# Optimization experiments

Measured on AMD Instinct MI355X. Metric: run time of the kernel, lower is better.

Reference implementation:

```python
import jax, jax.numpy as jnp
import numpy as np

H, C = 4, 128          # heads, hidden_channels
HC = H * C             # 512
F_IN = 9               # node_feat_dim
G_DIM = 50             # global_feat_dim (20 + 30 MACCS)
N = 30000              # nodes
E = 240000             # edges (before self-loops)
B = 64                 # graphs
EPS_BN = 1e-5
SLOPE = 0.2            # GATv2 LeakyReLU negative slope


def _glorot(key, shape):
    fan_in, fan_out = shape[0], shape[-1]
    lim = (6.0 / (fan_in + fan_out)) ** 0.5
    return jax.random.uniform(key, shape, jnp.float32, -lim, lim)


def setup_inputs() -> dict:
    key = jax.random.key(0)
    ks = jax.random.split(key, 20)
    x = jax.random.normal(ks[0], (N, F_IN), jnp.float32)
    global_feat = jax.random.normal(ks[1], (B, G_DIM), jnp.float32)
    edge_index = jax.random.randint(ks[2], (2, E), 0, N, jnp.int64) if jax.config.jax_enable_x64 else jax.random.randint(ks[2], (2, E), 0, N, jnp.int32)
    batch = jnp.sort(jax.random.randint(ks[3], (N,), 0, B, edge_index.dtype))
    return {
        "x": x, "global_feat": global_feat,
        # GATv2 layer 1
        "W1l": _glorot(ks[4], (F_IN, HC)), "b1l": jnp.zeros((HC,), jnp.float32),
        "W1r": _glorot(ks[5], (F_IN, HC)), "b1r": jnp.zeros((HC,), jnp.float32),
        "att1": _glorot(ks[6], (1, H, C))[0], "bias1": jnp.zeros((HC,), jnp.float32),
        # GATv2 layer 2
        "W2l": _glorot(ks[7], (HC, HC)), "b2l": jnp.zeros((HC,), jnp.float32),
        "W2r": _glorot(ks[8], (HC, HC)), "b2r": jnp.zeros((HC,), jnp.float32),
        "att2": _glorot(ks[9], (1, H, C))[0], "bias2": jnp.zeros((HC,), jnp.float32),
        # BatchNorms
        "bn1_g": jnp.ones((HC,), jnp.float32), "bn1_b": jnp.zeros((HC,), jnp.float32),
        "bn2_g": jnp.ones((HC,), jnp.float32), "bn2_b": jnp.zeros((HC,), jnp.float32),
        # MLP head
        "fc1_w": _glorot(ks[10], (HC + G_DIM, C)), "fc1_b": jnp.zeros((C,), jnp.float32),
        "fc2_w": _glorot(ks[11], (C, 1)), "fc2_b": jnp.zeros((1,), jnp.float32),
        "edge_index": edge_index, "batch": batch,
    }


def gatv2_layer(x, src, dst, Wl, bl, Wr, br, att, bias):
    n = x.shape[0]
    xl = (x @ Wl + bl).reshape(n, H, C)   # source transform
    xr = (x @ Wr + br).reshape(n, H, C)   # target transform
    m = xl[src] + xr[dst]                 # [E, H, C] gathered messages
    e = jnp.sum(jax.nn.leaky_relu(m, SLOPE) * att, axis=-1)  # [E, H]
    # segment softmax over edges grouped by target node
    e_max = jax.ops.segment_max(e, dst, num_segments=n)
    p = jnp.exp(e - e_max[dst])
    denom = jax.ops.segment_sum(p, dst, num_segments=n)
    alpha = p / (denom[dst] + 1e-16)      # [E, H]
    out = jax.ops.segment_sum(alpha[:, :, None] * xl[src], dst, num_segments=n)
    return out.reshape(n, HC) + bias


def batchnorm(x, g, b):
    mu = jnp.mean(x, axis=0)
    var = jnp.mean((x - mu) ** 2, axis=0)  # biased var (torch BN train mode)
    return (x - mu) * jax.lax.rsqrt(var + EPS_BN) * g + b


def reference(x, global_feat, W1l, b1l, W1r, b1r, att1, bias1,
              W2l, b2l, W2r, b2r, att2, bias2,
              bn1_g, bn1_b, bn2_g, bn2_b,
              fc1_w, fc1_b, fc2_w, fc2_b, edge_index, batch):
    n = x.shape[0]
    # add self-loops (PyG GATv2 default)
    loops = jnp.arange(n, dtype=edge_index.dtype)
    src = jnp.concatenate([edge_index[0], loops])
    dst = jnp.concatenate([edge_index[1], loops])

    h = gatv2_layer(x, src, dst, W1l, b1l, W1r, b1r, att1, bias1)
    h = jax.nn.relu(batchnorm(h, bn1_g, bn1_b))
    h = gatv2_layer(h, src, dst, W2l, b2l, W2r, b2r, att2, bias2)
    h = jax.nn.relu(batchnorm(h, bn2_g, bn2_b))

    # global mean pool over graphs
    sums = jax.ops.segment_sum(h, batch, num_segments=B)
    counts = jax.ops.segment_sum(jnp.ones((n, 1), h.dtype), batch, num_segments=B)
    pooled = sums / jnp.maximum(counts, 1.0)

    z = jnp.concatenate([pooled, global_feat], axis=1)
    z = jax.nn.relu(z @ fc1_w + fc1_b)  # dropout is identity in eval
    return jnp.squeeze(z @ fc2_w + fc2_b, axis=-1)
```

## Files before the change

kernel.cpp:

```cpp
#include <hip/hip_runtime.h>
#include <math.h>

#define NHEAD 4
#define CCH 128
#define HCD 512
#define SLOPE 0.2f
#define EPS_BN 1e-5f

typedef short s8v __attribute__((ext_vector_type(8)));
typedef float f32x4 __attribute__((ext_vector_type(4)));

__device__ __forceinline__ unsigned short f2bf(float f) {
    unsigned int u = __float_as_uint(f);
    return (unsigned short)((u + 0x7FFFu + ((u >> 16) & 1u)) >> 16);
}
__device__ __forceinline__ float bf2f(unsigned short b) {
    return __uint_as_float(((unsigned int)b) << 16);
}

__global__ void lin1_kernel(const float* __restrict__ x,
                            const float* __restrict__ Wl, const float* __restrict__ bl,
                            const float* __restrict__ Wr, const float* __restrict__ br,
                            float* __restrict__ xl, float* __restrict__ xr, int n) {
    int gid = blockIdx.x * blockDim.x + threadIdx.x;
    if (gid >= n * HCD) return;
    int node = gid >> 9;
    int c = gid & (HCD - 1);
    const float* xrow = x + node * 9;
    float a = bl[c], bz = br[c];
#pragma unroll
    for (int k = 0; k < 9; ++k) {
        float xv = xrow[k];
        a  = fmaf(xv, Wl[k * HCD + c], a);
        bz = fmaf(xv, Wr[k * HCD + c], bz);
    }
    xl[gid] = a;
    xr[gid] = bz;
}

__global__ void splitA_kernel(const float* __restrict__ h,
                              const float* __restrict__ scale, const float* __restrict__ shift,
                              unsigned short* __restrict__ Ah, unsigned short* __restrict__ Al,
                              int total4) {
    int gid = blockIdx.x * blockDim.x + threadIdx.x;
    if (gid >= total4) return;
    int c4 = gid & 127;
    float4 v = ((const float4*)h)[gid];
    float4 sc = ((const float4*)scale)[c4];
    float4 sh = ((const float4*)shift)[c4];
    float f0 = fmaxf(fmaf(v.x, sc.x, sh.x), 0.f);
    float f1 = fmaxf(fmaf(v.y, sc.y, sh.y), 0.f);
    float f2 = fmaxf(fmaf(v.z, sc.z, sh.z), 0.f);
    float f3 = fmaxf(fmaf(v.w, sc.w, sh.w), 0.f);
    unsigned short h0 = f2bf(f0), h1 = f2bf(f1), h2 = f2bf(f2), h3 = f2bf(f3);
    short4 hv = make_short4((short)h0, (short)h1, (short)h2, (short)h3);
    short4 lv = make_short4((short)f2bf(f0 - bf2f(h0)), (short)f2bf(f1 - bf2f(h1)),
                            (short)f2bf(f2 - bf2f(h2)), (short)f2bf(f3 - bf2f(h3)));
    ((short4*)Ah)[gid] = hv;
    ((short4*)Al)[gid] = lv;
}

__global__ void splitBT_kernel(const float* __restrict__ Wl, const float* __restrict__ Wr,
                               unsigned short* __restrict__ BThl, unsigned short* __restrict__ BTll,
                               unsigned short* __restrict__ BThr, unsigned short* __restrict__ BTlr) {
    int gid = blockIdx.x * blockDim.x + threadIdx.x;
    int col = gid >> 9;
    int k = gid & 511;
    float vl = Wl[k * HCD + col];
    float vr = Wr[k * HCD + col];
    unsigned short hl = f2bf(vl);
    unsigned short hr = f2bf(vr);
    BThl[gid] = hl; BTll[gid] = f2bf(vl - bf2f(hl));
    BThr[gid] = hr; BTlr[gid] = f2bf(vr - bf2f(hr));
}

__global__ __launch_bounds__(256) void gemm_mfma_kernel(
        const unsigned short* __restrict__ Ah, const unsigned short* __restrict__ Al,
        const unsigned short* __restrict__ BThL, const unsigned short* __restrict__ BTlL,
        const unsigned short* __restrict__ BThR, const unsigned short* __restrict__ BTlR,
        const float* __restrict__ biasl, const float* __restrict__ biasr,
        float* __restrict__ outL, float* __restrict__ outR, int M) {
    __shared__ short sAh[4096], sAl[4096], sBh[4096], sBl[4096];
    const int nrt = gridDim.x >> 3;
    const int bphys = blockIdx.x;
    const int l = (bphys & 7) * nrt + (bphys >> 3);
    const int y = l & 7;
    const int row0 = (l >> 3) * 128;
    const unsigned short* BTh = (y < 4) ? BThL : BThR;
    const unsigned short* BTl = (y < 4) ? BTlL : BTlR;
    const float* bias = (y < 4) ? biasl : biasr;
    float* C = (y < 4) ? outL : outR;
    const int col0 = (y & 3) * 128;
    const int tid  = threadIdx.x;
    const int wave = tid >> 6;
    const int lane = tid & 63;
    const int str = tid >> 2;
    const int skb = tid & 3;

    f32x4 acc[4][4];
#pragma unroll
    for (int i = 0; i < 4; ++i)
#pragma unroll
        for (int j = 0; j < 4; ++j) acc[i][j] = (f32x4){0.f, 0.f, 0.f, 0.f};

    const int abase = (wave & 1) * 2048;
    const int bbase = (wave >> 1) * 2048;
    const int rkb = lane >> 4;
    const int rrow = (lane & 15) ^ (rkb << 1);
    const int roff = rkb * 128 + rrow * 8;

    s8v pAh[2], pAl[2], pBh[2], pBl[2];
    const s8v zero8 = (s8v){0,0,0,0,0,0,0,0};

#define GLOAD(k0)                                                                     \
    {                                                                                 \
        _Pragma("unroll")                                                             \
        for (int cc = 0; cc < 2; ++cc) {                                              \
            int r = str + cc * 64;                                                    \
            if (row0 + r < M) {                                                       \
                pAh[cc] = *(const s8v*)(Ah + (size_t)(row0 + r) * 512 + (k0) + skb * 8); \
                pAl[cc] = *(const s8v*)(Al + (size_t)(row0 + r) * 512 + (k0) + skb * 8); \
            } else { pAh[cc] = zero8; pAl[cc] = zero8; }                              \
            pBh[cc] = *(const s8v*)(BTh + (size_t)(col0 + r) * 512 + (k0) + skb * 8); \
            pBl[cc] = *(const s8v*)(BTl + (size_t)(col0 + r) * 512 + (k0) + skb * 8); \
        }                                                                             \
    }

    GLOAD(0);
    for (int k0 = 0; k0 < 512; k0 += 32) {
        __syncthreads();
#pragma unroll
        for (int cc = 0; cc < 2; ++cc) {
            int r = str + cc * 64;
            int idx = (r >> 4) * 512 + skb * 128 + (((r & 15) ^ (skb << 1)) * 8);
            *(s8v*)&sAh[idx] = pAh[cc];
            *(s8v*)&sAl[idx] = pAl[cc];
            *(s8v*)&sBh[idx] = pBh[cc];
            *(s8v*)&sBl[idx] = pBl[cc];
        }
        __syncthreads();
        if (k0 + 32 < 512) GLOAD(k0 + 32);
#pragma unroll
        for (int sr = 0; sr < 4; ++sr) {
            s8v ah = *(const s8v*)&sAh[abase + sr * 512 + roff];
            s8v al = *(const s8v*)&sAl[abase + sr * 512 + roff];
#pragma unroll
            for (int sc = 0; sc < 4; ++sc) {
                s8v bh = *(const s8v*)&sBh[bbase + sc * 512 + roff];
                s8v bl = *(const s8v*)&sBl[bbase + sc * 512 + roff];
                acc[sr][sc] = __builtin_amdgcn_mfma_f32_16x16x32_bf16(ah, bh, acc[sr][sc], 0, 0, 0);
                acc[sr][sc] = __builtin_amdgcn_mfma_f32_16x16x32_bf16(al, bh, acc[sr][sc], 0, 0, 0);
                acc[sr][sc] = __builtin_amdgcn_mfma_f32_16x16x32_bf16(ah, bl, acc[sr][sc], 0, 0, 0);
            }
        }
    }
#undef GLOAD
    const int crow = row0 + (wave & 1) * 64;
    const int ccol = col0 + (wave >> 1) * 64;
#pragma unroll
    for (int sr = 0; sr < 4; ++sr) {
        int rbase = crow + sr * 16 + ((lane >> 4) << 2);
#pragma unroll
        for (int sc = 0; sc < 4; ++sc) {
            int col = ccol + sc * 16 + (lane & 15);
            float bb = bias[col];
#pragma unroll
            for (int j = 0; j < 4; ++j) {
                int r = rbase + j;
                if (r < M) C[(size_t)r * 512 + col] = acc[sr][sc][j] + bb;
            }
        }
    }
}


__global__ void hist_kernel(const int* __restrict__ edst, int* __restrict__ deg, int E, int Etot) {
    int e = blockIdx.x * blockDim.x + threadIdx.x;
    if (e >= Etot) return;
    int dst = (e < E) ? edst[e] : (e - E);
    atomicAdd(&deg[dst], 1);
}

__global__ __launch_bounds__(1024) void scan_kernel(const int* __restrict__ deg,
                                                    int* __restrict__ rowstart, int n) {
    __shared__ int buf[1024];
    __shared__ int carry;
    if (threadIdx.x == 0) carry = 0;
    __syncthreads();
    for (int base = 0; base < n; base += 1024) {
        int i = base + (int)threadIdx.x;
        int v = (i < n) ? deg[i] : 0;
        buf[threadIdx.x] = v;
        __syncthreads();
        for (int off = 1; off < 1024; off <<= 1) {
            int t = (threadIdx.x >= (unsigned)off) ? buf[threadIdx.x - off] : 0;
            __syncthreads();
            buf[threadIdx.x] += t;
            __syncthreads();
        }
        if (i < n) rowstart[i] = carry + buf[threadIdx.x] - v;
        int blocksum = buf[1023];
        __syncthreads();
        if (threadIdx.x == 0) carry += blocksum;
        __syncthreads();
    }
    if (threadIdx.x == 0) rowstart[n] = carry;
}

__global__ void scatter_kernel(const int* __restrict__ esrc, const int* __restrict__ edst,
                               const int* __restrict__ rowstart, int* __restrict__ cursor,
                               int* __restrict__ s_src, int E, int Etot) {
    int e = blockIdx.x * blockDim.x + threadIdx.x;
    if (e >= Etot) return;
    int src = (e < E) ? esrc[e] : (e - E);
    int dst = (e < E) ? edst[e] : (e - E);
    int pos = rowstart[dst] + atomicAdd(&cursor[dst], 1);
    s_src[pos] = src;
}

__global__ __launch_bounds__(256) void gat_fused_kernel(
        const float* __restrict__ xl, const float* __restrict__ xr,
        const float* __restrict__ att,
        const int* __restrict__ rowstart, const int* __restrict__ s_src,
        float* __restrict__ out) {
    int node = blockIdx.x;
    int h    = threadIdx.x >> 6;
    int lane = threadIdx.x & 63;
    int beg = rowstart[node];
    int end = rowstart[node + 1];
    int c0 = h * CCH + (lane << 1);
    float2 r2 = *(const float2*)(xr + (size_t)node * HCD + c0);
    float2 a2 = *(const float2*)(att + c0);
    float m = -3.0e38f, den = 0.f, acc0 = 0.f, acc1 = 0.f;

    int j = beg;
    float2 q0, q1, q2, q3;
    q0 = *(const float2*)(xl + (size_t)s_src[j] * HCD + c0);
    if (j + 1 < end) q1 = *(const float2*)(xl + (size_t)s_src[j + 1] * HCD + c0);
    if (j + 2 < end) q2 = *(const float2*)(xl + (size_t)s_src[j + 2] * HCD + c0);
    if (j + 3 < end) q3 = *(const float2*)(xl + (size_t)s_src[j + 3] * HCD + c0);

    while (j + 1 < end) {
        float2 A = q0, B = q1;
        q0 = q2; q1 = q3;
        if (j + 4 < end) q2 = *(const float2*)(xl + (size_t)s_src[j + 4] * HCD + c0);
        if (j + 5 < end) q3 = *(const float2*)(xl + (size_t)s_src[j + 5] * HCD + c0);
        float ta0 = A.x + r2.x; ta0 = (ta0 > 0.f) ? ta0 : SLOPE * ta0;
        float ta1 = A.y + r2.y; ta1 = (ta1 > 0.f) ? ta1 : SLOPE * ta1;
        float tb0 = B.x + r2.x; tb0 = (tb0 > 0.f) ? tb0 : SLOPE * tb0;
        float tb1 = B.y + r2.y; tb1 = (tb1 > 0.f) ? tb1 : SLOPE * tb1;
        float sA = fmaf(ta0, a2.x, ta1 * a2.y);
        float sB = fmaf(tb0, a2.x, tb1 * a2.y);
#pragma unroll
        for (int k = 1; k < 64; k <<= 1) {
            sA += __shfl_xor(sA, k);
            sB += __shfl_xor(sB, k);
        }
        float mn = fmaxf(m, fmaxf(sA, sB));
        float sc = expf(m - mn);
        float pA = expf(sA - mn);
        float pB = expf(sB - mn);
        den  = fmaf(den,  sc, pA + pB);
        acc0 = fmaf(acc0, sc, fmaf(pA, A.x, pB * B.x));
        acc1 = fmaf(acc1, sc, fmaf(pA, A.y, pB * B.y));
        m = mn;
        j += 2;
    }
    if (j < end) {
        float2 A = q0;
        float ta0 = A.x + r2.x; ta0 = (ta0 > 0.f) ? ta0 : SLOPE * ta0;
        float ta1 = A.y + r2.y; ta1 = (ta1 > 0.f) ? ta1 : SLOPE * ta1;
        float sA = fmaf(ta0, a2.x, ta1 * a2.y);
#pragma unroll
        for (int k = 1; k < 64; k <<= 1) sA += __shfl_xor(sA, k);
        float mn = fmaxf(m, sA);
        float sc = expf(m - mn);
        float pA = expf(sA - mn);
        den  = fmaf(den,  sc, pA);
        acc0 = fmaf(acc0, sc, pA * A.x);
        acc1 = fmaf(acc1, sc, pA * A.y);
    }
    float inv = 1.0f / (den + 1e-16f);
    *(float2*)(out + (size_t)node * HCD + c0) = make_float2(acc0 * inv, acc1 * inv);
}

__global__ void bn_stats_kernel(const float* __restrict__ h, float* __restrict__ sum,
                                float* __restrict__ sumsq, int n) {
    int c = blockIdx.y * blockDim.x + threadIdx.x;
    int r0 = blockIdx.x * 128;
    int r1 = min(r0 + 128, n);
    float s = 0.f, s2 = 0.f;
    for (int r = r0; r < r1; ++r) {
        float v = h[(size_t)r * HCD + c];
        s += v;
        s2 = fmaf(v, v, s2);
    }
    atomicAdd(&sum[c], s);
    atomicAdd(&sumsq[c], s2);
}

__global__ void bn_finalize_kernel(const float* __restrict__ sum, const float* __restrict__ sumsq,
                                   const float* __restrict__ g, const float* __restrict__ b,
                                   float* __restrict__ scale, float* __restrict__ shift, int n) {
    int c = threadIdx.x;
    float inv_n = 1.0f / (float)n;
    float mu = sum[c] * inv_n;
    float var = fmaxf(sumsq[c] * inv_n - mu * mu, 0.0f);
    float sc = g[c] * rsqrtf(var + EPS_BN);
    scale[c] = sc;
    shift[c] = b[c] - mu * sc;
}

__device__ __forceinline__ int lower_bound_i(const int* __restrict__ a, int n, int key) {
    int lo = 0, hi = n;
    while (lo < hi) {
        int mid = (lo + hi) >> 1;
        if (a[mid] < key) lo = mid + 1; else hi = mid;
    }
    return lo;
}

__global__ void pool_bnrelu_kernel(const float* __restrict__ h, const int* __restrict__ batch,
                                   const float* __restrict__ scale, const float* __restrict__ shift,
                                   float* __restrict__ pooled, int n) {
    int g = blockIdx.x;
    int c = threadIdx.x;
    int start = lower_bound_i(batch, n, g);
    int end   = lower_bound_i(batch, n, g + 1);
    float sc = scale[c], sh = shift[c];
    float s = 0.f;
    for (int r = start; r < end; ++r)
        s += fmaxf(fmaf(h[(size_t)r * HCD + c], sc, sh), 0.f);
    float cnt = (float)max(end - start, 1);
    pooled[(size_t)g * HCD + c] = s / cnt;
}

__global__ void head_kernel(const float* __restrict__ pooled, const float* __restrict__ gfeat,
                            const float* __restrict__ fc1w, const float* __restrict__ fc1b,
                            const float* __restrict__ fc2w, const float* __restrict__ fc2b,
                            float* __restrict__ out, int gdim) {
    int g = blockIdx.x;
    int j = threadIdx.x;
    float acc = fc1b[j];
    const float* prow = pooled + (size_t)g * HCD;
    for (int i = 0; i < HCD; ++i) acc = fmaf(prow[i], fc1w[i * CCH + j], acc);
    const float* grow = gfeat + (size_t)g * gdim;
    for (int i = 0; i < gdim; ++i) acc = fmaf(grow[i], fc1w[(HCD + i) * CCH + j], acc);
    acc = fmaxf(acc, 0.f);
    __shared__ float z[CCH];
    z[j] = acc * fc2w[j];
    __syncthreads();
    for (int s = CCH / 2; s > 0; s >>= 1) {
        if (j < s) z[j] += z[j + s];
        __syncthreads();
    }
    if (j == 0) out[g] = z[0] + fc2b[0];
}

extern "C" void kernel_launch(void* const* d_in, const int* in_sizes, int n_in,
                              void* d_out, int out_size, void* d_ws, size_t ws_size,
                              hipStream_t stream) {
    const float* x     = (const float*)d_in[0];
    const float* gfeat = (const float*)d_in[1];
    const float* W1l   = (const float*)d_in[2];
    const float* b1l   = (const float*)d_in[3];
    const float* W1r   = (const float*)d_in[4];
    const float* b1r   = (const float*)d_in[5];
    const float* att1  = (const float*)d_in[6];
    const float* W2l   = (const float*)d_in[8];
    const float* b2l   = (const float*)d_in[9];
    const float* W2r   = (const float*)d_in[10];
    const float* b2r   = (const float*)d_in[11];
    const float* att2  = (const float*)d_in[12];
    const float* bn1_g = (const float*)d_in[14];
    const float* bn1_b = (const float*)d_in[15];
    const float* bn2_g = (const float*)d_in[16];
    const float* bn2_b = (const float*)d_in[17];
    const float* fc1w  = (const float*)d_in[18];
    const float* fc1b  = (const float*)d_in[19];
    const float* fc2w  = (const float*)d_in[20];
    const float* fc2b  = (const float*)d_in[21];
    const int* eidx    = (const int*)d_in[22];
    const int* batch   = (const int*)d_in[23];

    const int n    = in_sizes[0] / 9;
    const int E    = in_sizes[22] / 2;
    const int Etot = E + n;
    const int b    = out_size;
    const int gdim = in_sizes[1] / b;
    const int* esrc = eidx;
    const int* edst = eidx + E;

    float* ws = (float*)d_ws;
    size_t nHC = (size_t)n * HCD;
    float* xl      = ws;
    float* xr      = xl + nHC;
    float* hbuf    = xr + nHC;
    int* deg       = (int*)(hbuf + nHC);
    int* rowstart  = deg + n;
    int* cursor    = rowstart + n + 1;
    int* s_src     = cursor + n;
    float* bnsum   = (float*)(s_src + Etot);
    float* bnsumsq = bnsum + HCD;
    float* bnscale = bnsumsq + HCD;
    float* bnshift = bnscale + HCD;
    float* pooled  = bnshift + HCD;
    unsigned short* Ah   = (unsigned short*)(pooled + (size_t)b * HCD);
    unsigned short* Al   = Ah + nHC;
    unsigned short* BThl = Al + nHC;
    unsigned short* BTll = BThl + HCD * HCD;
    unsigned short* BThr = BTll + HCD * HCD;
    unsigned short* BTlr = BThr + HCD * HCD;

    const int BLK = 256;
    const int linBlocks  = (int)((nHC + BLK - 1) / BLK);
    const int eBlocks    = (Etot + BLK - 1) / BLK;
    const int bnxBlocks  = (n + 127) / 128;
    const int saBlocks   = (int)((nHC / 4 + BLK - 1) / BLK);
    const int nrt        = (n + 127) / 128;
    dim3 gemmGrid(nrt * 8);

    hipMemsetAsync(deg, 0, (size_t)(2 * n + 1) * sizeof(int), stream);
    hipMemsetAsync(cursor, 0, (size_t)n * sizeof(int), stream);
    hist_kernel<<<eBlocks, BLK, 0, stream>>>(edst, deg, E, Etot);
    scan_kernel<<<1, 1024, 0, stream>>>(deg, rowstart, n);
    scatter_kernel<<<eBlocks, BLK, 0, stream>>>(esrc, edst, rowstart, cursor, s_src, E, Etot);
    splitBT_kernel<<<(HCD * HCD) / BLK, BLK, 0, stream>>>(W2l, W2r, BThl, BTll, BThr, BTlr);

    lin1_kernel<<<linBlocks, BLK, 0, stream>>>(x, W1l, b1l, W1r, b1r, xl, xr, n);
    gat_fused_kernel<<<n, 256, 0, stream>>>(xl, xr, att1, rowstart, s_src, hbuf);
    hipMemsetAsync(bnsum, 0, HCD * 2 * sizeof(float), stream);
    bn_stats_kernel<<<dim3(bnxBlocks, 2), BLK, 0, stream>>>(hbuf, bnsum, bnsumsq, n);
    bn_finalize_kernel<<<1, HCD, 0, stream>>>(bnsum, bnsumsq, bn1_g, bn1_b, bnscale, bnshift, n);

    splitA_kernel<<<saBlocks, BLK, 0, stream>>>(hbuf, bnscale, bnshift, Ah, Al, (int)(nHC / 4));
    gemm_mfma_kernel<<<gemmGrid, BLK, 0, stream>>>(Ah, Al, BThl, BTll, BThr, BTlr,
                                                   b2l, b2r, xl, xr, n);
    gat_fused_kernel<<<n, 256, 0, stream>>>(xl, xr, att2, rowstart, s_src, hbuf);
    hipMemsetAsync(bnsum, 0, HCD * 2 * sizeof(float), stream);
    bn_stats_kernel<<<dim3(bnxBlocks, 2), BLK, 0, stream>>>(hbuf, bnsum, bnsumsq, n);
    bn_finalize_kernel<<<1, HCD, 0, stream>>>(bnsum, bnsumsq, bn2_g, bn2_b, bnscale, bnshift, n);

    pool_bnrelu_kernel<<<b, HCD, 0, stream>>>(hbuf, batch, bnscale, bnshift, pooled, n);
    head_kernel<<<b, CCH, 0, stream>>>(pooled, gfeat, fc1w, fc1b, fc2w, fc2b, (float*)d_out, gdim);
}
```

Measured before the change: 861.7 us.

## Double-buffer LDS tiles in split-bf16 MFMA GEMM to drop a barrier per k-step

Shared-memory tiles for the hi/lo A and B operands are now double-buffered. Each k-step writes the next tile into the alternate buffer after its MFMAs and issues the global prefetch two tiles ahead. This leaves one __syncthreads per iteration instead of two. The cost is that LDS per block doubles to 64 KB, which may limit how many blocks can reside on a CU, and register pressure rises because the prefetch runs further ahead.

```diff
diff --git a/kernel.cpp b/kernel.cpp
--- a/kernel.cpp
+++ b/kernel.cpp
@@ -80,7 +80,7 @@
         const unsigned short* __restrict__ BThR, const unsigned short* __restrict__ BTlR,
         const float* __restrict__ biasl, const float* __restrict__ biasr,
         float* __restrict__ outL, float* __restrict__ outR, int M) {
-    __shared__ short sAh[4096], sAl[4096], sBh[4096], sBl[4096];
+    __shared__ short sAh[2][4096], sAl[2][4096], sBh[2][4096], sBl[2][4096];
     const int nrt = gridDim.x >> 3;
     const int bphys = blockIdx.x;
     const int l = (bphys & 7) * nrt + (bphys >> 3);
@@ -126,35 +126,47 @@
         }                                                                             \
     }
 
+#define LSTORE(buf)                                                                   \
+    {                                                                                 \
+        _Pragma("unroll")                                                             \
+        for (int cc = 0; cc < 2; ++cc) {                                              \
+            int r = str + cc * 64;                                                    \
+            int idx = (r >> 4) * 512 + skb * 128 + (((r & 15) ^ (skb << 1)) * 8);     \
+            *(s8v*)&sAh[buf][idx] = pAh[cc];                                          \
+            *(s8v*)&sAl[buf][idx] = pAl[cc];                                          \
+            *(s8v*)&sBh[buf][idx] = pBh[cc];                                          \
+            *(s8v*)&sBl[buf][idx] = pBl[cc];                                          \
+        }                                                                             \
+    }
+
     GLOAD(0);
+    LSTORE(0);
+    GLOAD(32);
+    __syncthreads();
+
     for (int k0 = 0; k0 < 512; k0 += 32) {
-        __syncthreads();
-#pragma unroll
-        for (int cc = 0; cc < 2; ++cc) {
-            int r = str + cc * 64;
-            int idx = (r >> 4) * 512 + skb * 128 + (((r & 15) ^ (skb << 1)) * 8);
-            *(s8v*)&sAh[idx] = pAh[cc];
-            *(s8v*)&sAl[idx] = pAl[cc];
-            *(s8v*)&sBh[idx] = pBh[cc];
-            *(s8v*)&sBl[idx] = pBl[cc];
-        }
-        __syncthreads();
-        if (k0 + 32 < 512) GLOAD(k0 + 32);
+        const int cur = (k0 >> 5) & 1;
 #pragma unroll
         for (int sr = 0; sr < 4; ++sr) {
-            s8v ah = *(const s8v*)&sAh[abase + sr * 512 + roff];
-            s8v al = *(const s8v*)&sAl[abase + sr * 512 + roff];
+            s8v ah = *(const s8v*)&sAh[cur][abase + sr * 512 + roff];
+            s8v al = *(const s8v*)&sAl[cur][abase + sr * 512 + roff];
 #pragma unroll
             for (int sc = 0; sc < 4; ++sc) {
-                s8v bh = *(const s8v*)&sBh[bbase + sc * 512 + roff];
-                s8v bl = *(const s8v*)&sBl[bbase + sc * 512 + roff];
+                s8v bh = *(const s8v*)&sBh[cur][bbase + sc * 512 + roff];
+                s8v bl = *(const s8v*)&sBl[cur][bbase + sc * 512 + roff];
                 acc[sr][sc] = __builtin_amdgcn_mfma_f32_16x16x32_bf16(ah, bh, acc[sr][sc], 0, 0, 0);
                 acc[sr][sc] = __builtin_amdgcn_mfma_f32_16x16x32_bf16(al, bh, acc[sr][sc], 0, 0, 0);
                 acc[sr][sc] = __builtin_amdgcn_mfma_f32_16x16x32_bf16(ah, bl, acc[sr][sc], 0, 0, 0);
             }
         }
+        if (k0 + 32 < 512) {
+            LSTORE(cur ^ 1);
+            if (k0 + 64 < 512) GLOAD(k0 + 64);
+            __syncthreads();
+        }
     }
 #undef GLOAD
+#undef LSTORE
     const int crow = row0 + (wave & 1) * 64;
     const int ccol = col0 + (wave >> 1) * 64;
 #pragma unroll
```

Result: no change. 870.6 us (+1.0%).
